# Performance work log

Hardware: AMD Instinct MI355X
Metric: run time of the kernel (lower is better)

## Reference

```python
import jax, jax.numpy as jnp
import numpy as np

HIDDEN = 4096
NH = 32          # query heads
NKV = 2          # kv heads (multi_query_group_num)
HD = 128         # head dim
ROT = HD // 2    # GLM style: rotary applied to first half of head_dim
THETA = 10000.0
SCALE = HD ** -0.5
G = NH // NKV    # query heads per kv group


def _glm_rope(x, positions):
    # x: [B, S, N, HD]; GPT-J interleaved rotation on the first ROT dims.
    inv_freq = 1.0 / (THETA ** (jnp.arange(0, ROT, 2, dtype=jnp.float32) / ROT))  # [ROT//2]
    ang = positions.astype(jnp.float32)[..., None] * inv_freq                      # [B, S, ROT//2]
    cos = jnp.cos(ang)[:, :, None, :]
    sin = jnp.sin(ang)[:, :, None, :]
    xr, xp = x[..., :ROT], x[..., ROT:]
    x1, x2 = xr[..., 0::2], xr[..., 1::2]
    r1 = x1 * cos - x2 * sin
    r2 = x1 * sin + x2 * cos
    xr = jnp.stack([r1, r2], axis=-1).reshape(xr.shape)  # re-interleave
    return jnp.concatenate([xr, xp], axis=-1)


def setup_inputs() -> dict:
    key = jax.random.key(0)
    k1, k2, k3, k4 = jax.random.split(key, 4)
    B, S = 2, 2048
    positions = jnp.broadcast_to(jnp.arange(S, dtype=jnp.int64), (B, S))
    hidden_states = jax.random.normal(k1, (B, S, HIDDEN), dtype=jnp.float32)
    qkv_out = NH * HD + 2 * NKV * HD  # 4608
    w_qkv = jax.random.normal(k2, (qkv_out, HIDDEN), dtype=jnp.float32) * 0.02
    b_qkv = jax.random.normal(k3, (qkv_out,), dtype=jnp.float32) * 0.02
    w_dense = jax.random.normal(k4, (HIDDEN, NH * HD), dtype=jnp.float32) * 0.02
    return {"positions": positions, "hidden_states": hidden_states,
            "w_qkv": w_qkv, "b_qkv": b_qkv, "w_dense": w_dense}


def reference(positions, hidden_states, w_qkv, b_qkv, w_dense):
    B, S, _ = hidden_states.shape
    mixed = hidden_states @ w_qkv.T + b_qkv                      # [B,S,4608]
    q = mixed[..., : NH * HD].reshape(B, S, NH, HD)
    k = mixed[..., NH * HD: NH * HD + NKV * HD].reshape(B, S, NKV, HD)
    v = mixed[..., NH * HD + NKV * HD:].reshape(B, S, NKV, HD)

    q = _glm_rope(q, positions)
    k = _glm_rope(k, positions)

    # GQA: view q as [B, S, NKV, G, HD]
    qg = q.reshape(B, S, NKV, G, HD)
    scores = jnp.einsum('bqkgd,bskd->bkgqs', qg, k) * SCALE      # [B,NKV,G,S,S]
    causal = jnp.tril(jnp.ones((S, S), dtype=bool))
    scores = jnp.where(causal, scores, jnp.finfo(scores.dtype).min)
    probs = jax.nn.softmax(scores, axis=-1)
    ctx = jnp.einsum('bkgqs,bskd->bqkgd', probs, v)              # [B,S,NKV,G,HD]
    ctx = ctx.reshape(B, S, NH * HD)
    return ctx @ w_dense.T                                       # [B,S,HIDDEN]
```

## Files before the change

kernel.cpp:

```cpp
#include <hip/hip_runtime.h>

typedef float f32x4 __attribute__((ext_vector_type(4)));
typedef __bf16 bf16x8 __attribute__((ext_vector_type(8)));
typedef unsigned short u16x4 __attribute__((ext_vector_type(4)));
typedef unsigned short u16x8 __attribute__((ext_vector_type(8)));

#define HIDDEN 4096
#define NH 32
#define NKV 2
#define HD 128
#define SLEN 2048
#define BATCH 2
#define QKV_OUT 4608
#define MROWS 4096
#define ATT_SCALE 0.08838834764831845f
#define KCHUNK 1024

__device__ __forceinline__ unsigned short f2bf(float f) {
  unsigned int u = __float_as_uint(f);
  u += 0x7fffu + ((u >> 16) & 1u);
  return (unsigned short)(u >> 16);
}

__device__ __forceinline__ float bf2f(unsigned short s) {
  return __uint_as_float((unsigned int)s << 16);
}

__device__ __forceinline__ void gload16(const void* g, void* l) {
  __builtin_amdgcn_global_load_lds((const __attribute__((address_space(1))) void*)g,
                                   (__attribute__((address_space(3))) void*)l, 16, 0, 0);
}

__global__ __launch_bounds__(256) void cvt3_f32_bf16(
    const float* __restrict__ s0, unsigned short* __restrict__ d0, int n0,
    const float* __restrict__ s1, unsigned short* __restrict__ d1, int n1,
    const float* __restrict__ s2, unsigned short* __restrict__ d2, int n2) {
  const int ntot = n0 + n1 + n2;
  const int stride = gridDim.x * blockDim.x;
  for (int i = blockIdx.x * blockDim.x + threadIdx.x; i < ntot; i += stride) {
    const float* src;
    unsigned short* dst;
    int j = i;
    if (j < n0) { src = s0; dst = d0; }
    else if (j < n0 + n1) { j -= n0; src = s1; dst = d1; }
    else { j -= n0 + n1; src = s2; dst = d2; }
    float4 v = reinterpret_cast<const float4*>(src)[j];
    u16x4 o;
    o[0] = f2bf(v.x); o[1] = f2bf(v.y); o[2] = f2bf(v.z); o[3] = f2bf(v.w);
    reinterpret_cast<u16x4*>(dst)[j] = o;
  }
}

__global__ __launch_bounds__(256) void build_trig(float2* __restrict__ tab) {
  const int idx = blockIdx.x * 256 + threadIdx.x;
  const int p = idx >> 5, j = idx & 31;
  const float inv = __expf(-(float)j * 0.28782313662425572f);
  float sn, cs;
  sincosf((float)p * inv, &sn, &cs);
  tab[idx] = make_float2(cs, sn);
}

__global__ __launch_bounds__(512) void gemm_bf16_mfma(
    const unsigned short* __restrict__ A, const unsigned short* __restrict__ B,
    const float* __restrict__ bias, void* __restrict__ Cout, int M, int N, int K,
    int mode, const float2* __restrict__ tab, const int* __restrict__ positions,
    unsigned short* __restrict__ Qb, unsigned short* __restrict__ Kb,
    unsigned short* __restrict__ Vt) {
  __shared__ unsigned short as_[128 * 64];
  __shared__ unsigned short bs_[256 * 64];
  const int tid = threadIdx.x;
  const int wave = tid >> 6;
  const int lane = tid & 63;
  const int lr = lane & 15, lg = lane >> 4;
  const int m0 = blockIdx.y * 128;
  const int n0 = blockIdx.x * 256;
  const int wm = (wave >> 2) * 64;
  const int wn = (wave & 3) * 64;

  f32x4 acc[4][4] = {};

  const int srow8 = tid >> 3;
  const int schunk = (tid & 7) ^ (srow8 & 7);
  const int scol = schunk * 8;
  unsigned short* lA = as_ + wave * 512;
  unsigned short* lB = bs_ + wave * 512;

  const int nk = K >> 6;
  for (int kt = 0; kt < nk; ++kt) {
    const int kb = kt << 6;
    __syncthreads();
    gload16(A + (size_t)(m0 + srow8) * K + kb + scol, lA);
    gload16(A + (size_t)(m0 + 64 + srow8) * K + kb + scol, lA + 4096);
    gload16(B + (size_t)(n0 + srow8) * K + kb + scol, lB);
    gload16(B + (size_t)(n0 + 64 + srow8) * K + kb + scol, lB + 4096);
    gload16(B + (size_t)(n0 + 128 + srow8) * K + kb + scol, lB + 8192);
    gload16(B + (size_t)(n0 + 192 + srow8) * K + kb + scol, lB + 12288);
    __syncthreads();

#pragma unroll
    for (int kk = 0; kk < 2; ++kk) {
      bf16x8 aF[4], bF[4];
#pragma unroll
      for (int m4 = 0; m4 < 4; ++m4)
        aF[m4] = *reinterpret_cast<const bf16x8*>(
            &as_[(wm + m4 * 16 + lr) * 64 + (((kk * 4 + lg) ^ (lr & 7)) << 3)]);
#pragma unroll
      for (int n4 = 0; n4 < 4; ++n4)
        bF[n4] = *reinterpret_cast<const bf16x8*>(
            &bs_[(wn + n4 * 16 + lr) * 64 + (((kk * 4 + lg) ^ (lr & 7)) << 3)]);
#pragma unroll
      for (int m4 = 0; m4 < 4; ++m4)
#pragma unroll
        for (int n4 = 0; n4 < 4; ++n4)
          acc[m4][n4] =
              __builtin_amdgcn_mfma_f32_16x16x32_bf16(aF[m4], bF[n4], acc[m4][n4], 0, 0, 0);
    }
  }

  if (mode == 0) {
    float* C = (float*)Cout;
#pragma unroll
    for (int m4 = 0; m4 < 4; ++m4) {
#pragma unroll
      for (int n4 = 0; n4 < 4; ++n4) {
        const int col = n0 + wn + n4 * 16 + lr;
        const float bv = bias ? bias[col] : 0.0f;
#pragma unroll
        for (int r = 0; r < 4; ++r) {
          const int row = m0 + wm + m4 * 16 + lg * 4 + r;
          C[(size_t)row * N + col] = acc[m4][n4][r] + bv;
        }
      }
    }
  } else {
#pragma unroll
    for (int m4 = 0; m4 < 4; ++m4) {
      const int rowb = m0 + wm + m4 * 16 + lg * 4;
      const int bb = rowb >> 11;
      const int ss = rowb & 2047;
      int pos[4];
#pragma unroll
      for (int r = 0; r < 4; ++r) pos[r] = positions[rowb + r];
#pragma unroll
      for (int n4 = 0; n4 < 4; ++n4) {
        const int col = n0 + wn + n4 * 16 + lr;
        const float bv = bias[col];
        float val[4];
#pragma unroll
        for (int r = 0; r < 4; ++r) val[r] = acc[m4][n4][r] + bv;
        const int d = col & 127;
        const bool isv = (col >= NH * HD + NKV * HD);
        const bool isq = (col < NH * HD);
        if (d < 64 && !isv) {
          const int j = d >> 1;
#pragma unroll
          for (int r = 0; r < 4; ++r) {
            const float2 t = tab[pos[r] * 32 + j];
            const float other = __shfl_xor(val[r], 1);
            val[r] = (col & 1) ? (other * t.y + val[r] * t.x)
                               : (val[r] * t.x - other * t.y);
          }
        }
        if (isq) {
          const int hh = col >> 7;
          unsigned short* q = Qb + ((size_t)(bb * NH + hh) * SLEN + ss) * HD + d;
#pragma unroll
          for (int r = 0; r < 4; ++r) q[(size_t)r * HD] = f2bf(val[r] * ATT_SCALE);
        } else if (!isv) {
          const int kvh = (col - NH * HD) >> 7;
          unsigned short* k = Kb + ((size_t)(bb * NKV + kvh) * SLEN + ss) * HD + d;
#pragma unroll
          for (int r = 0; r < 4; ++r) k[(size_t)r * HD] = f2bf(val[r]);
        } else {
          const int kvh = (col - NH * HD - NKV * HD) >> 7;
          u16x4 o;
#pragma unroll
          for (int r = 0; r < 4; ++r) o[r] = f2bf(val[r]);
          *reinterpret_cast<u16x4*>(
              &Vt[((size_t)(bb * NKV + kvh) * HD + d) * SLEN + ss]) = o;
        }
      }
    }
  }
}

__global__ __launch_bounds__(512) void flash_mfma(const unsigned short* __restrict__ Qb,
                                                  const unsigned short* __restrict__ Kb,
                                                  const unsigned short* __restrict__ Vt,
                                                  unsigned short* __restrict__ ctx,
                                                  unsigned short* __restrict__ Om,
                                                  float* __restrict__ Ml) {
  __shared__ unsigned short Ks[2][64 * 128];
  __shared__ unsigned short Vs[128 * 64];
  __shared__ unsigned short Ps[8][16 * 64];

  const int tid = threadIdx.x;
  const int wave = tid >> 6, lane = tid & 63;
  const int lr = lane & 15, lg = lane >> 4;

  const int i = blockIdx.x;
  int qt, c;
  if (i < 8) { qt = 15 - i; c = 0; }
  else if (i < 16) { qt = 23 - i; c = 1; }
  else { qt = 23 - i; c = 0; }
  const int h = blockIdx.y, b = blockIdx.z;
  const int kv = h >> 4;
  const int q0 = qt * 128;
  const int s_begin = c * KCHUNK;
  const int s_end = min(KCHUNK * (c + 1), q0 + 128);
  const int nkt = (s_end - s_begin) >> 6;
  const bool single = (c == 0) && (s_end == q0 + 128);
  const int qbw = q0 + wave * 16;

  const unsigned short* Kbase = Kb + (size_t)(b * NKV + kv) * SLEN * HD;
  const unsigned short* Vbase = Vt + (size_t)(b * NKV + kv) * HD * SLEN;

  bf16x8 bQ[4];
  {
    const unsigned short* qp = Qb + ((size_t)(b * NH + h) * SLEN + qbw + lr) * HD;
#pragma unroll
    for (int ks = 0; ks < 4; ++ks)
      bQ[ks] = *reinterpret_cast<const bf16x8*>(qp + lg * 8 + ks * 32);
  }

  f32x4 accO[8] = {};
  float mi = -1e30f, li = 0.0f;

  const int vrow_off = lane >> 3, vchunk = lane & 7;
#define STAGE_K(cb, t)                                                                  \
  {                                                                                     \
    const int ss = s_begin + (t) * 64;                                                  \
    _Pragma("unroll") for (int si = 0; si < 2; ++si) {                                  \
      const int krow = wave * 8 + si * 4 + lg;                                          \
      gload16(Kbase + (size_t)(ss + krow) * HD + ((lr ^ (krow & 7)) << 3),              \
              &Ks[cb][(wave * 8 + si * 4) * 128]);                                      \
    }                                                                                   \
  }
#define STAGE_V(t)                                                                      \
  {                                                                                     \
    const int ss = s_begin + (t) * 64;                                                  \
    _Pragma("unroll") for (int si = 0; si < 2; ++si) {                                  \
      const int drow = wave * 16 + si * 8 + vrow_off;                                   \
      gload16(Vbase + (size_t)drow * SLEN + ss + ((vchunk ^ (drow & 7)) << 3),          \
              &Vs[(wave * 16 + si * 8) * 64]);                                          \
    }                                                                                   \
  }

  STAGE_K(0, 0);
  __syncthreads();

  unsigned short* Pw = Ps[wave];

  for (int kt = 0; kt < nkt; ++kt) {
    const int cur = kt & 1;
    const int s0 = s_begin + kt * 64;
    STAGE_V(kt);
    if (kt + 1 < nkt) STAGE_K(cur ^ 1, kt + 1);
    const bool part = (s0 < qbw + 16);

    f32x4 accS[4] = {};
    if (part) {
      bf16x8 aK[4][4];
#pragma unroll
      for (int kb = 0; kb < 4; ++kb)
#pragma unroll
        for (int ks = 0; ks < 4; ++ks)
          aK[kb][ks] = *reinterpret_cast<const bf16x8*>(
              &Ks[cur][(kb * 16 + lr) * 128 + (((ks * 4 + lg) ^ (lr & 7)) << 3)]);
#pragma unroll
      for (int kb = 0; kb < 4; ++kb)
#pragma unroll
        for (int ks = 0; ks < 4; ++ks)
          accS[kb] = __builtin_amdgcn_mfma_f32_16x16x32_bf16(aK[kb][ks], bQ[ks], accS[kb], 0, 0, 0);
    }

    __syncthreads();

    if (part) {
      const int qrow = qbw + lr;
      float v[16];
#pragma unroll
      for (int kb = 0; kb < 4; ++kb)
#pragma unroll
        for (int r = 0; r < 4; ++r) v[kb * 4 + r] = accS[kb][r];
      if (s0 + 63 > qbw) {
#pragma unroll
        for (int kb = 0; kb < 4; ++kb)
#pragma unroll
          for (int r = 0; r < 4; ++r)
            if (s0 + kb * 16 + lg * 4 + r > qrow) v[kb * 4 + r] = -1e30f;
      }
      float m16 = v[0];
#pragma unroll
      for (int i2 = 1; i2 < 16; ++i2) m16 = fmaxf(m16, v[i2]);
      m16 = fmaxf(m16, __shfl_xor(m16, 16));
      m16 = fmaxf(m16, __shfl_xor(m16, 32));
      const float mnew = fmaxf(mi, m16);
      const float cf = __expf(mi - mnew);
      mi = mnew;
      float rs = 0.0f;
#pragma unroll
      for (int i2 = 0; i2 < 16; ++i2) {
        const float p = __expf(v[i2] - mnew);
        v[i2] = p;
        rs += p;
      }
      rs += __shfl_xor(rs, 16);
      rs += __shfl_xor(rs, 32);
      li = li * cf + rs;
#pragma unroll
      for (int n8 = 0; n8 < 8; ++n8) accO[n8] *= cf;
#pragma unroll
      for (int kb = 0; kb < 4; ++kb) {
        const int slot = (kb * 2 + (lg >> 1)) ^ (lr & 7);
        u16x4 pk;
        pk[0] = f2bf(v[kb * 4 + 0]); pk[1] = f2bf(v[kb * 4 + 1]);
        pk[2] = f2bf(v[kb * 4 + 2]); pk[3] = f2bf(v[kb * 4 + 3]);
        *reinterpret_cast<u16x4*>(&Pw[lr * 64 + slot * 8 + (lg & 1) * 4]) = pk;
      }

      bf16x8 pa[2];
#pragma unroll
      for (int ks = 0; ks < 2; ++ks)
        pa[ks] = *reinterpret_cast<const bf16x8*>(
            &Pw[lr * 64 + (((ks * 4 + lg) ^ (lr & 7)) << 3)]);
#pragma unroll
      for (int ks = 0; ks < 2; ++ks) {
#pragma unroll
        for (int n8 = 0; n8 < 8; ++n8) {
          bf16x8 aV = *reinterpret_cast<const bf16x8*>(
              &Vs[(n8 * 16 + lr) * 64 + (((ks * 4 + lg) ^ (lr & 7)) << 3)]);
          accO[n8] = __builtin_amdgcn_mfma_f32_16x16x32_bf16(aV, pa[ks], accO[n8], 0, 0, 0);
        }
      }
    }

    __syncthreads();
  }
#undef STAGE_K
#undef STAGE_V

  if (single) {
    const float inv = 1.0f / li;
    unsigned short* orow =
        ctx + (size_t)(b * SLEN + qbw + lr) * HIDDEN + h * HD + lg * 4;
#pragma unroll
    for (int n8 = 0; n8 < 8; ++n8) {
      u16x4 o;
#pragma unroll
      for (int r = 0; r < 4; ++r) o[r] = f2bf(accO[n8][r] * inv);
      *reinterpret_cast<u16x4*>(orow + n8 * 16) = o;
    }
  } else {
    const int row1k = qbw + lr - 1024;
    const size_t pbase = (size_t)((b * NH + h) * 2 + c) * 1024 + row1k;
    if (lg == 0) {
      Ml[pbase * 2] = mi;
      Ml[pbase * 2 + 1] = li;
    }
    unsigned short* prow = Om + pbase * 128 + lg * 4;
#pragma unroll
    for (int n8 = 0; n8 < 8; ++n8) {
      u16x4 o;
#pragma unroll
      for (int r = 0; r < 4; ++r) o[r] = f2bf(accO[n8][r]);
      *reinterpret_cast<u16x4*>(prow + n8 * 16) = o;
    }
  }
}

__global__ __launch_bounds__(256) void combine_partials(
    const unsigned short* __restrict__ Om, const float* __restrict__ Ml,
    unsigned short* __restrict__ ctx) {
  const int g = blockIdx.x * 64 + (threadIdx.x >> 2);
  const int p = threadIdx.x & 3;
  const int row1k = g & 1023;
  const int h = (g >> 10) & 31;
  const int b = g >> 15;
  const size_t base0 = (size_t)((b * NH + h) * 2 + 0) * 1024 + row1k;
  const size_t base1 = (size_t)((b * NH + h) * 2 + 1) * 1024 + row1k;
  const float m0 = Ml[base0 * 2], l0 = Ml[base0 * 2 + 1];
  const float m1 = Ml[base1 * 2], l1 = Ml[base1 * 2 + 1];
  const float mx = fmaxf(m0, m1);
  const float w0 = __expf(m0 - mx), w1 = __expf(m1 - mx);
  const float inv = 1.0f / (w0 * l0 + w1 * l1);
  const unsigned short* n0 = Om + base0 * 128 + p * 32;
  const unsigned short* n1 = Om + base1 * 128 + p * 32;
  unsigned short* orow =
      ctx + (size_t)(b * SLEN + 1024 + row1k) * HIDDEN + h * HD + p * 32;
#pragma unroll
  for (int cch = 0; cch < 4; ++cch) {
    u16x8 a = *reinterpret_cast<const u16x8*>(n0 + cch * 8);
    u16x8 d = *reinterpret_cast<const u16x8*>(n1 + cch * 8);
    u16x8 o;
#pragma unroll
    for (int j = 0; j < 8; ++j)
      o[j] = f2bf((w0 * bf2f(a[j]) + w1 * bf2f(d[j])) * inv);
    *reinterpret_cast<u16x8*>(orow + cch * 8) = o;
  }
}

extern "C" void kernel_launch(void* const* d_in, const int* in_sizes, int n_in,
                              void* d_out, int out_size, void* d_ws, size_t ws_size,
                              hipStream_t stream) {
  const int* positions = (const int*)d_in[0];
  const float* hidden = (const float*)d_in[1];
  const float* w_qkv = (const float*)d_in[2];
  const float* b_qkv = (const float*)d_in[3];
  const float* w_dense = (const float*)d_in[4];
  float* out = (float*)d_out;

  char* ws = (char*)d_ws;
  size_t off = 0;
  unsigned short* mixed = (unsigned short*)(ws + off);
  off += (size_t)MROWS * QKV_OUT * 4;
  unsigned short* h_bf = (unsigned short*)(ws + off);
  off += (size_t)MROWS * HIDDEN * 2;
  unsigned short* wq_bf = (unsigned short*)(ws + off);
  off += (size_t)QKV_OUT * HIDDEN * 2;
  unsigned short* wd_bf = (unsigned short*)(ws + off);
  off += (size_t)HIDDEN * HIDDEN * 2;
  unsigned short* Kb = (unsigned short*)(ws + off);
  off += (size_t)BATCH * NKV * SLEN * HD * 2;
  unsigned short* Vt = (unsigned short*)(ws + off);
  off += (size_t)BATCH * NKV * SLEN * HD * 2;
  float2* trig = (float2*)(ws + off);
  off += (size_t)2048 * 32 * 8;
  unsigned short* Qb = h_bf;
  Qb = mixed;
  unsigned short* ctx_bf = mixed + (size_t)MROWS * HIDDEN;
  unsigned short* Om = wq_bf;
  float* Ml = (float*)(ws + off);
  off += (size_t)BATCH * NH * 2 * 1024 * 2 * 4;

  cvt3_f32_bf16<<<2048, 256, 0, stream>>>(hidden, h_bf, MROWS * HIDDEN / 4,
                                          w_qkv, wq_bf, QKV_OUT * HIDDEN / 4,
                                          w_dense, wd_bf, HIDDEN * HIDDEN / 4);
  build_trig<<<256, 256, 0, stream>>>(trig);

  gemm_bf16_mfma<<<dim3(QKV_OUT / 256, MROWS / 128), 512, 0, stream>>>(
      h_bf, wq_bf, b_qkv, nullptr, MROWS, QKV_OUT, HIDDEN, 2, trig, positions,
      Qb, Kb, Vt);

  flash_mfma<<<dim3(24, NH, BATCH), 512, 0, stream>>>(Qb, Kb, Vt, ctx_bf, Om, Ml);

  combine_partials<<<1024, 256, 0, stream>>>(Om, Ml, ctx_bf);

  gemm_bf16_mfma<<<dim3(HIDDEN / 256, MROWS / 128), 512, 0, stream>>>(
      ctx_bf, wd_bf, nullptr, out, MROWS, HIDDEN, HIDDEN, 0, nullptr, nullptr,
      nullptr, nullptr, nullptr);
}
```

Before: 529.4 us.

## Double-buffer GEMM with 256x256 tiles, phased MFMA schedule, and fuse trig table build

```diff
diff --git a/kernel.cpp b/kernel.cpp
--- a/kernel.cpp
+++ b/kernel.cpp
@@ -34,7 +34,16 @@
 __global__ __launch_bounds__(256) void cvt3_f32_bf16(
     const float* __restrict__ s0, unsigned short* __restrict__ d0, int n0,
     const float* __restrict__ s1, unsigned short* __restrict__ d1, int n1,
-    const float* __restrict__ s2, unsigned short* __restrict__ d2, int n2) {
+    const float* __restrict__ s2, unsigned short* __restrict__ d2, int n2,
+    float2* __restrict__ tab) {
+  if (blockIdx.x < 256) {
+    const int idx = blockIdx.x * 256 + threadIdx.x;
+    const int p = idx >> 5, j = idx & 31;
+    const float inv = __expf(-(float)j * 0.28782313662425572f);
+    float sn, cs;
+    sincosf((float)p * inv, &sn, &cs);
+    tab[idx] = make_float2(cs, sn);
+  }
   const int ntot = n0 + n1 + n2;
   const int stride = gridDim.x * blockDim.x;
   for (int i = blockIdx.x * blockDim.x + threadIdx.x; i < ntot; i += stride) {
@@ -51,136 +60,180 @@
   }
 }
 
-__global__ __launch_bounds__(256) void build_trig(float2* __restrict__ tab) {
-  const int idx = blockIdx.x * 256 + threadIdx.x;
-  const int p = idx >> 5, j = idx & 31;
-  const float inv = __expf(-(float)j * 0.28782313662425572f);
-  float sn, cs;
-  sincosf((float)p * inv, &sn, &cs);
-  tab[idx] = make_float2(cs, sn);
-}
-
-__global__ __launch_bounds__(512) void gemm_bf16_mfma(
+__global__ __launch_bounds__(512, 2) void gemm_bf16_mfma(
     const unsigned short* __restrict__ A, const unsigned short* __restrict__ B,
     const float* __restrict__ bias, void* __restrict__ Cout, int M, int N, int K,
     int mode, const float2* __restrict__ tab, const int* __restrict__ positions,
     unsigned short* __restrict__ Qb, unsigned short* __restrict__ Kb,
     unsigned short* __restrict__ Vt) {
-  __shared__ unsigned short as_[128 * 64];
-  __shared__ unsigned short bs_[256 * 64];
+  __shared__ unsigned short as_[2][256 * 64];
+  __shared__ unsigned short bs_[2][256 * 64];
   const int tid = threadIdx.x;
   const int wave = tid >> 6;
   const int lane = tid & 63;
   const int lr = lane & 15, lg = lane >> 4;
-  const int m0 = blockIdx.y * 128;
+  const int m0 = blockIdx.y * 256;
   const int n0 = blockIdx.x * 256;
-  const int wm = (wave >> 2) * 64;
+  const int wm = (wave >> 2) * 128;
   const int wn = (wave & 3) * 64;
 
-  f32x4 acc[4][4] = {};
+  f32x4 acc[2][4][2][2] = {};
+  bf16x8 aF[4][2], bF[2][2];
 
   const int srow8 = tid >> 3;
-  const int schunk = (tid & 7) ^ (srow8 & 7);
-  const int scol = schunk * 8;
-  unsigned short* lA = as_ + wave * 512;
-  unsigned short* lB = bs_ + wave * 512;
-
-  const int nk = K >> 6;
-  for (int kt = 0; kt < nk; ++kt) {
-    const int kb = kt << 6;
-    __syncthreads();
-    gload16(A + (size_t)(m0 + srow8) * K + kb + scol, lA);
-    gload16(A + (size_t)(m0 + 64 + srow8) * K + kb + scol, lA + 4096);
-    gload16(B + (size_t)(n0 + srow8) * K + kb + scol, lB);
-    gload16(B + (size_t)(n0 + 64 + srow8) * K + kb + scol, lB + 4096);
-    gload16(B + (size_t)(n0 + 128 + srow8) * K + kb + scol, lB + 8192);
-    gload16(B + (size_t)(n0 + 192 + srow8) * K + kb + scol, lB + 12288);
-    __syncthreads();
-
-#pragma unroll
-    for (int kk = 0; kk < 2; ++kk) {
-      bf16x8 aF[4], bF[4];
-#pragma unroll
-      for (int m4 = 0; m4 < 4; ++m4)
-        aF[m4] = *reinterpret_cast<const bf16x8*>(
-            &as_[(wm + m4 * 16 + lr) * 64 + (((kk * 4 + lg) ^ (lr & 7)) << 3)]);
-#pragma unroll
-      for (int n4 = 0; n4 < 4; ++n4)
-        bF[n4] = *reinterpret_cast<const bf16x8*>(
-            &bs_[(wn + n4 * 16 + lr) * 64 + (((kk * 4 + lg) ^ (lr & 7)) << 3)]);
-#pragma unroll
-      for (int m4 = 0; m4 < 4; ++m4)
-#pragma unroll
-        for (int n4 = 0; n4 < 4; ++n4)
-          acc[m4][n4] =
-              __builtin_amdgcn_mfma_f32_16x16x32_bf16(aF[m4], bF[n4], acc[m4][n4], 0, 0, 0);
-    }
-  }
+  const int scol = ((tid & 7) ^ (srow8 & 7)) * 8;
+
+#define GS_A(cb, t, h)                                                          \
+  {                                                                             \
+    const int kb_ = (t) << 6;                                                   \
+    gload16(A + (size_t)(m0 + (h) * 128 + srow8) * K + kb_ + scol,              \
+            &as_[cb][((h) * 128 + wave * 8) * 64]);                             \
+    gload16(A + (size_t)(m0 + (h) * 128 + 64 + srow8) * K + kb_ + scol,         \
+            &as_[cb][((h) * 128 + 64 + wave * 8) * 64]);                        \
+  }
+#define GS_B(cb, t, h)                                                          \
+  {                                                                             \
+    const int kb_ = (t) << 6;                                                   \
+    gload16(B + (size_t)(n0 + (h) * 128 + srow8) * K + kb_ + scol,              \
+            &bs_[cb][((h) * 128 + wave * 8) * 64]);                             \
+    gload16(B + (size_t)(n0 + (h) * 128 + 64 + srow8) * K + kb_ + scol,         \
+            &bs_[cb][((h) * 128 + 64 + wave * 8) * 64]);                        \
+  }
+#define RD_A(cb, MH)                                                            \
+  _Pragma("unroll") for (int mf = 0; mf < 4; ++mf)                              \
+  _Pragma("unroll") for (int kk = 0; kk < 2; ++kk)                              \
+      aF[mf][kk] = *reinterpret_cast<const bf16x8*>(                            \
+          &as_[cb][(wm + (MH) * 64 + mf * 16 + lr) * 64 +                       \
+                   (((kk * 4 + lg) ^ (lr & 7)) << 3)]);
+#define RD_B(cb, NH)                                                            \
+  _Pragma("unroll") for (int nf = 0; nf < 2; ++nf)                              \
+  _Pragma("unroll") for (int kk = 0; kk < 2; ++kk)                              \
+      bF[nf][kk] = *reinterpret_cast<const bf16x8*>(                            \
+          &bs_[cb][(wn + (NH) * 32 + nf * 16 + lr) * 64 +                       \
+                   (((kk * 4 + lg) ^ (lr & 7)) << 3)]);
+#define PH_MFMA(MH, NH)                                                         \
+  __builtin_amdgcn_s_setprio(1);                                                \
+  _Pragma("unroll") for (int kk = 0; kk < 2; ++kk)                              \
+  _Pragma("unroll") for (int mf = 0; mf < 4; ++mf)                              \
+  _Pragma("unroll") for (int nf = 0; nf < 2; ++nf)                              \
+      acc[MH][mf][NH][nf] = __builtin_amdgcn_mfma_f32_16x16x32_bf16(            \
+          aF[mf][kk], bF[nf][kk], acc[MH][mf][NH][nf], 0, 0, 0);                \
+  __builtin_amdgcn_s_setprio(0);
+#define BAR __builtin_amdgcn_s_barrier()
+#define LG0                                            \
+  asm volatile("s_waitcnt lgkmcnt(0)" ::: "memory");   \
+  __builtin_amdgcn_sched_barrier(0)
+#define VM0 asm volatile("s_waitcnt vmcnt(0)" ::: "memory")
+
+  const int niter = K >> 7;
+
+  GS_A(0, 0, 0); GS_A(0, 0, 1); GS_B(0, 0, 0); GS_B(0, 0, 1);
+  VM0;
+  BAR;
+
+  for (int i = 0; i < niter; ++i) {
+    const int tO = 2 * i + 1;
+    const bool more = (i + 1) < niter;
+    RD_A(0, 0); RD_B(0, 0); GS_A(1, tO, 0);
+    BAR; LG0; PH_MFMA(0, 0); BAR;
+    RD_B(0, 1); GS_A(1, tO, 1);
+    BAR; LG0; PH_MFMA(0, 1); BAR;
+    RD_A(0, 1); GS_B(1, tO, 0);
+    BAR; LG0; PH_MFMA(1, 1); BAR;
+    RD_B(0, 0); GS_B(1, tO, 1);
+    BAR; LG0; PH_MFMA(1, 0);
+    VM0;
+    BAR;
+    RD_A(1, 0); RD_B(1, 0); if (more) GS_A(0, tO + 1, 0);
+    BAR; LG0; PH_MFMA(0, 0); BAR;
+    RD_B(1, 1); if (more) GS_A(0, tO + 1, 1);
+    BAR; LG0; PH_MFMA(0, 1); BAR;
+    RD_A(1, 1); if (more) GS_B(0, tO + 1, 0);
+    BAR; LG0; PH_MFMA(1, 1); BAR;
+    RD_B(1, 0); if (more) GS_B(0, tO + 1, 1);
+    BAR; LG0; PH_MFMA(1, 0);
+    VM0;
+    BAR;
+  }
+#undef GS_A
+#undef GS_B
+#undef RD_A
+#undef RD_B
+#undef PH_MFMA
+#undef BAR
+#undef LG0
+#undef VM0
 
   if (mode == 0) {
     float* C = (float*)Cout;
 #pragma unroll
-    for (int m4 = 0; m4 < 4; ++m4) {
-#pragma unroll
-      for (int n4 = 0; n4 < 4; ++n4) {
-        const int col = n0 + wn + n4 * 16 + lr;
-        const float bv = bias ? bias[col] : 0.0f;
-#pragma unroll
-        for (int r = 0; r < 4; ++r) {
-          const int row = m0 + wm + m4 * 16 + lg * 4 + r;
-          C[(size_t)row * N + col] = acc[m4][n4][r] + bv;
-        }
+    for (int mh = 0; mh < 2; ++mh)
+#pragma unroll
+      for (int mf = 0; mf < 4; ++mf)
+#pragma unroll
+        for (int nh = 0; nh < 2; ++nh)
+#pragma unroll
+          for (int nf = 0; nf < 2; ++nf) {
+            const int col = n0 + wn + nh * 32 + nf * 16 + lr;
+            const float bv = bias ? bias[col] : 0.0f;
+            const int row = m0 + wm + mh * 64 + mf * 16 + lg * 4;
+#pragma unroll
+            for (int r = 0; r < 4; ++r)
+              C[(size_t)(row + r) * N + col] = acc[mh][mf][nh][nf][r] + bv;
+          }
+  } else {
+#pragma unroll
+    for (int mh = 0; mh < 2; ++mh)
+#pragma unroll
+      for (int mf = 0; mf < 4; ++mf) {
+        const int rowb = m0 + wm + mh * 64 + mf * 16 + lg * 4;
+        const int bb = rowb >> 11;
+        const int ss = rowb & 2047;
+        int pos[4];
+#pragma unroll
+        for (int r = 0; r < 4; ++r) pos[r] = positions[rowb + r];
+#pragma unroll
+        for (int nh = 0; nh < 2; ++nh)
+#pragma unroll
+          for (int nf = 0; nf < 2; ++nf) {
+            const int col = n0 + wn + nh * 32 + nf * 16 + lr;
+            const float bv = bias[col];
+            float val[4];
+#pragma unroll
+            for (int r = 0; r < 4; ++r) val[r] = acc[mh][mf][nh][nf][r] + bv;
+            const int d = col & 127;
+            const bool isv = (col >= NH * HD + NKV * HD);
+            const bool isq = (col < NH * HD);
+            if (d < 64 && !isv) {
+              const int j = d >> 1;
+#pragma unroll
+              for (int r = 0; r < 4; ++r) {
+                const float2 t = tab[pos[r] * 32 + j];
+                const float other = __shfl_xor(val[r], 1);
+                val[r] = (col & 1) ? (other * t.y + val[r] * t.x)
+                                   : (val[r] * t.x - other * t.y);
+              }
+            }
+            if (isq) {
+              const int hh = col >> 7;
+              unsigned short* q = Qb + ((size_t)(bb * NH + hh) * SLEN + ss) * HD + d;
+#pragma unroll
+              for (int r = 0; r < 4; ++r) q[(size_t)r * HD] = f2bf(val[r] * ATT_SCALE);
+            } else if (!isv) {
+              const int kvh = (col - NH * HD) >> 7;
+              unsigned short* k = Kb + ((size_t)(bb * NKV + kvh) * SLEN + ss) * HD + d;
+#pragma unroll
+              for (int r = 0; r < 4; ++r) k[(size_t)r * HD] = f2bf(val[r]);
+            } else {
+              const int kvh = (col - NH * HD - NKV * HD) >> 7;
+              u16x4 o;
+#pragma unroll
+              for (int r = 0; r < 4; ++r) o[r] = f2bf(val[r]);
+              *reinterpret_cast<u16x4*>(
+                  &Vt[((size_t)(bb * NKV + kvh) * HD + d) * SLEN + ss]) = o;
+            }
+          }
       }
-    }
-  } else {
-#pragma unroll
-    for (int m4 = 0; m4 < 4; ++m4) {
-      const int rowb = m0 + wm + m4 * 16 + lg * 4;
-      const int bb = rowb >> 11;
-      const int ss = rowb & 2047;
-      int pos[4];
-#pragma unroll
-      for (int r = 0; r < 4; ++r) pos[r] = positions[rowb + r];
-#pragma unroll
-      for (int n4 = 0; n4 < 4; ++n4) {
-        const int col = n0 + wn + n4 * 16 + lr;
-        const float bv = bias[col];
-        float val[4];
-#pragma unroll
-        for (int r = 0; r < 4; ++r) val[r] = acc[m4][n4][r] + bv;
-        const int d = col & 127;
-        const bool isv = (col >= NH * HD + NKV * HD);
-        const bool isq = (col < NH * HD);
-        if (d < 64 && !isv) {
-          const int j = d >> 1;
-#pragma unroll
-          for (int r = 0; r < 4; ++r) {
-            const float2 t = tab[pos[r] * 32 + j];
-            const float other = __shfl_xor(val[r], 1);
-            val[r] = (col & 1) ? (other * t.y + val[r] * t.x)
-                               : (val[r] * t.x - other * t.y);
-          }
-        }
-        if (isq) {
-          const int hh = col >> 7;
-          unsigned short* q = Qb + ((size_t)(bb * NH + hh) * SLEN + ss) * HD + d;
-#pragma unroll
-          for (int r = 0; r < 4; ++r) q[(size_t)r * HD] = f2bf(val[r] * ATT_SCALE);
-        } else if (!isv) {
-          const int kvh = (col - NH * HD) >> 7;
-          unsigned short* k = Kb + ((size_t)(bb * NKV + kvh) * SLEN + ss) * HD + d;
-#pragma unroll
-          for (int r = 0; r < 4; ++r) k[(size_t)r * HD] = f2bf(val[r]);
-        } else {
-          const int kvh = (col - NH * HD - NKV * HD) >> 7;
-          u16x4 o;
-#pragma unroll
-          for (int r = 0; r < 4; ++r) o[r] = f2bf(val[r]);
-          *reinterpret_cast<u16x4*>(
-              &Vt[((size_t)(bb * NKV + kvh) * HD + d) * SLEN + ss]) = o;
-        }
-      }
-    }
   }
 }
 
@@ -426,19 +479,17 @@
   off += (size_t)BATCH * NKV * SLEN * HD * 2;
   float2* trig = (float2*)(ws + off);
   off += (size_t)2048 * 32 * 8;
-  unsigned short* Qb = h_bf;
-  Qb = mixed;
+  float* Ml = (float*)(ws + off);
+  off += (size_t)BATCH * NH * 2 * 1024 * 2 * 4;
+  unsigned short* Qb = mixed;
   unsigned short* ctx_bf = mixed + (size_t)MROWS * HIDDEN;
   unsigned short* Om = wq_bf;
-  float* Ml = (float*)(ws + off);
-  off += (size_t)BATCH * NH * 2 * 1024 * 2 * 4;
 
   cvt3_f32_bf16<<<2048, 256, 0, stream>>>(hidden, h_bf, MROWS * HIDDEN / 4,
                                           w_qkv, wq_bf, QKV_OUT * HIDDEN / 4,
-                                          w_dense, wd_bf, HIDDEN * HIDDEN / 4);
-  build_trig<<<256, 256, 0, stream>>>(trig);
-
-  gemm_bf16_mfma<<<dim3(QKV_OUT / 256, MROWS / 128), 512, 0, stream>>>(
+                                          w_dense, wd_bf, HIDDEN * HIDDEN / 4, trig);
+
+  gemm_bf16_mfma<<<dim3(QKV_OUT / 256, MROWS / 256), 512, 0, stream>>>(
       h_bf, wq_bf, b_qkv, nullptr, MROWS, QKV_OUT, HIDDEN, 2, trig, positions,
       Qb, Kb, Vt);
 
@@ -446,7 +497,7 @@
 
   combine_partials<<<1024, 256, 0, stream>>>(Om, Ml, ctx_bf);
 
-  gemm_bf16_mfma<<<dim3(HIDDEN / 256, MROWS / 128), 512, 0, stream>>>(
+  gemm_bf16_mfma<<<dim3(HIDDEN / 256, MROWS / 256), 512, 0, stream>>>(
       ctx_bf, wd_bf, nullptr, out, MROWS, HIDDEN, HIDDEN, 0, nullptr, nullptr,
       nullptr, nullptr, nullptr);
 }
```

Result: slower. 621.6 us (+17.4%).
